# Kernel optimization log

Hardware: AMD Instinct MI355X
Metric: run time of the kernel (lower is better)

The kernel has to match this reference:

```python
import jax, jax.numpy as jnp
import numpy as np

D_MODEL = 1024
H = 16
DK = 64
DV = 64
EPS = 1e-5


def setup_inputs() -> dict:
    key = jax.random.key(0)
    ks = jax.random.split(key, 12)
    B, NQ, NK = 4, 2048, 2048
    std = 0.001  # init.normal_(weight, std=0.001), biases zero
    return {
        "queries": jax.random.normal(ks[0], (B, NQ, D_MODEL), jnp.float32),
        "keys": jax.random.normal(ks[1], (B, NK, D_MODEL), jnp.float32),
        "values": jax.random.normal(ks[2], (B, NK, D_MODEL), jnp.float32),
        "attention_mask": jnp.ones((B, NK), jnp.int32),  # 1 = keep
        "Wq": jax.random.normal(ks[3], (D_MODEL, H * DK), jnp.float32) * std,
        "bq": jnp.zeros((H * DK,), jnp.float32),
        "Wk": jax.random.normal(ks[4], (D_MODEL, H * DK), jnp.float32) * std,
        "bk": jnp.zeros((H * DK,), jnp.float32),
        "Wv": jax.random.normal(ks[5], (D_MODEL, H * DV), jnp.float32) * std,
        "bv": jnp.zeros((H * DV,), jnp.float32),
        "Wo": jax.random.normal(ks[6], (H * DV, D_MODEL), jnp.float32) * std,
        "bo": jnp.zeros((D_MODEL,), jnp.float32),
        "gamma": jnp.ones((D_MODEL,), jnp.float32),
        "beta": jnp.zeros((D_MODEL,), jnp.float32),
    }


def reference(queries, keys, values, attention_mask, Wq, bq, Wk, bk, Wv, bv, Wo, bo, gamma, beta):
    b, nq, _ = queries.shape
    nk = keys.shape[1]
    q = (queries @ Wq + bq).reshape(b, nq, H, DK)   # (b, nq, h, dk)
    k = (keys @ Wk + bk).reshape(b, nk, H, DK)      # (b, nk, h, dk)
    v = (values @ Wv + bv).reshape(b, nk, H, DV)    # (b, nk, h, dv)
    scale = 1.0 / np.sqrt(DK).astype(np.float32)
    att = jnp.einsum('bqhd,bkhd->bhqk', q, k) * scale  # (b, h, nq, nk)
    mask = attention_mask[:, None, None, :].astype(bool)
    att = jnp.where(mask, att, -jnp.inf)
    att = jax.nn.softmax(att, axis=-1)
    # dropout is identity at inference
    out = jnp.einsum('bhqk,bkhd->bqhd', att, v).reshape(b, nq, H * DV)
    out = out @ Wo + bo
    x = out + queries  # residual
    mean = jnp.mean(x, axis=-1, keepdims=True)
    var = jnp.mean(jnp.square(x - mean), axis=-1, keepdims=True)
    return gamma * (x - mean) * jax.lax.rsqrt(var + EPS) + beta
```

## Files before the change

### kernel.cpp

```cpp
#include <hip/hip_runtime.h>

typedef __bf16 bf16x8 __attribute__((ext_vector_type(8)));
typedef __bf16 bf16x4 __attribute__((ext_vector_type(4)));
typedef float f32x4 __attribute__((ext_vector_type(4)));
typedef unsigned short u16;

#if __has_builtin(__builtin_amdgcn_exp2f)
#define EXP2(x) __builtin_amdgcn_exp2f(x)
#else
#define EXP2(x) exp2f(x)
#endif

__device__ __forceinline__ float bf2f(u16 u){
    union { unsigned int i; float f; } x; x.i = ((unsigned int)u) << 16; return x.f;
}
__device__ __forceinline__ u16 f2bf(float f){
    union { float f; unsigned int i; } x; x.f = f;
    unsigned int r = x.i + 0x7fff + ((x.i >> 16) & 1);
    return (u16)(r >> 16);
}
__device__ __forceinline__ int4 cvt8(const float4 a, const float4 b){
    union { u16 h[8]; int4 v; } u;
    u.h[0] = f2bf(a.x); u.h[1] = f2bf(a.y); u.h[2] = f2bf(a.z); u.h[3] = f2bf(a.w);
    u.h[4] = f2bf(b.x); u.h[5] = f2bf(b.y); u.h[6] = f2bf(b.z); u.h[7] = f2bf(b.w);
    return u.v;
}

__global__ __launch_bounds__(256) void transpose4(
    const float* __restrict__ w0, const float* __restrict__ w1,
    const float* __restrict__ w2, const float* __restrict__ w3,
    u16* __restrict__ out)
{
    __shared__ float tile[32][33];
    int mat = blockIdx.z;
    const float* in = (mat == 0) ? w0 : (mat == 1) ? w1 : (mat == 2) ? w2 : w3;
    u16* o = out + (size_t)mat * 1048576;
    int bx = blockIdx.x * 32, by = blockIdx.y * 32;
    int tx = threadIdx.x & 31, ty = threadIdx.x >> 5;
    #pragma unroll
    for (int i = 0; i < 32; i += 8)
        tile[ty + i][tx] = in[(size_t)(by + ty + i) * 1024 + bx + tx];
    __syncthreads();
    #pragma unroll
    for (int i = 0; i < 32; i += 8)
        o[(size_t)(bx + ty + i) * 1024 + by + tx] = f2bf(tile[tx][ty + i]);
}

template<int MODE, bool AF32>
__global__ __launch_bounds__(256) void gemm_bt(
    const void* __restrict__ Av, const u16* __restrict__ Bt,
    const float* __restrict__ bias, const float* __restrict__ resid,
    void* __restrict__ Cv, float scale)
{
    constexpr int K = 1024;
    __shared__ alignas(16) u16 As[2][128][32];
    __shared__ alignas(16) u16 Bs[2][128][32];
    const int tid = threadIdx.x;
    const int lane = tid & 63, wid = tid >> 6;
    const int wm = wid >> 1, wn = wid & 1;
    const int m0 = blockIdx.x * 128, n0 = blockIdx.y * 128;
    const int r0 = tid >> 2;
    const int kc = (tid & 3) * 8;
    const int fr = lane & 15, fk = (lane >> 4) * 8;

    const float* Af0 = (const float*)Av + (size_t)(m0 + r0) * K + kc;
    const float* Af1 = Af0 + (size_t)64 * K;
    const u16*   Ah0 = (const u16*)Av + (size_t)(m0 + r0) * K + kc;
    const u16*   Ah1 = Ah0 + (size_t)64 * K;
    const u16* Brow0 = Bt + (size_t)(n0 + r0) * K + kc;
    const u16* Brow1 = Brow0 + (size_t)64 * K;

    int4 pa0, pa1, pb0, pb1;
    if constexpr (AF32) {
        pa0 = cvt8(((const float4*)Af0)[0], ((const float4*)Af0)[1]);
        pa1 = cvt8(((const float4*)Af1)[0], ((const float4*)Af1)[1]);
    } else {
        pa0 = *(const int4*)(Ah0);
        pa1 = *(const int4*)(Ah1);
    }
    pb0 = *(const int4*)(Brow0);
    pb1 = *(const int4*)(Brow1);
    *(int4*)&As[0][r0][kc]      = pa0;
    *(int4*)&As[0][r0 + 64][kc] = pa1;
    *(int4*)&Bs[0][r0][kc]      = pb0;
    *(int4*)&Bs[0][r0 + 64][kc] = pb1;
    __syncthreads();

    f32x4 acc[4][4] = {};
    constexpr int NT = K / 32;
    for (int t = 0; t < NT; ++t) {
        int cur = t & 1, nxt = cur ^ 1;
        if (t + 1 < NT) {
            if constexpr (AF32) {
                pa0 = cvt8(((const float4*)(Af0 + (t + 1) * 32))[0],
                           ((const float4*)(Af0 + (t + 1) * 32))[1]);
                pa1 = cvt8(((const float4*)(Af1 + (t + 1) * 32))[0],
                           ((const float4*)(Af1 + (t + 1) * 32))[1]);
            } else {
                pa0 = *(const int4*)(Ah0 + (t + 1) * 32);
                pa1 = *(const int4*)(Ah1 + (t + 1) * 32);
            }
            pb0 = *(const int4*)(Brow0 + (t + 1) * 32);
            pb1 = *(const int4*)(Brow1 + (t + 1) * 32);
        }
        bf16x8 af[4], bfr[4];
        #pragma unroll
        for (int i = 0; i < 4; i++) {
            af[i]  = *(const bf16x8*)&As[cur][wm * 64 + i * 16 + fr][fk];
            bfr[i] = *(const bf16x8*)&Bs[cur][wn * 64 + i * 16 + fr][fk];
        }
        #pragma unroll
        for (int mi = 0; mi < 4; mi++)
            #pragma unroll
            for (int ni = 0; ni < 4; ni++)
                acc[mi][ni] = __builtin_amdgcn_mfma_f32_16x16x32_bf16(
                    af[mi], bfr[ni], acc[mi][ni], 0, 0, 0);
        if (t + 1 < NT) {
            *(int4*)&As[nxt][r0][kc]      = pa0;
            *(int4*)&As[nxt][r0 + 64][kc] = pa1;
            *(int4*)&Bs[nxt][r0][kc]      = pb0;
            *(int4*)&Bs[nxt][r0 + 64][kc] = pb1;
        }
        __syncthreads();
    }

    #pragma unroll
    for (int ni = 0; ni < 4; ni++) {
        int col = n0 + wn * 64 + ni * 16 + fr;
        float bcol = bias[col];
        #pragma unroll
        for (int mi = 0; mi < 4; mi++) {
            #pragma unroll
            for (int r = 0; r < 4; r++) {
                int m = m0 + wm * 64 + mi * 16 + (lane >> 4) * 4 + r;
                float val = acc[mi][ni][r] + bcol;
                if (MODE == 2) {
                    val += resid[(size_t)m * 1024 + col];
                    ((float*)Cv)[(size_t)m * 1024 + col] = val;
                } else {
                    val *= scale;
                    int b = m >> 11, q = m & 2047;
                    int h = col >> 6, d = col & 63;
                    size_t base = (size_t)(b * 16 + h) * 131072;
                    if (MODE == 0) ((u16*)Cv)[base + (size_t)q * 64 + d] = f2bf(val);
                    else           ((u16*)Cv)[base + (size_t)d * 2048 + q] = f2bf(val);
                }
            }
        }
    }
}

__global__ __launch_bounds__(256) void attn_k(
    const u16* __restrict__ Qp, const u16* __restrict__ Kp,
    const u16* __restrict__ Vt, const int* __restrict__ mask,
    u16* __restrict__ O)
{
    __shared__ alignas(16) u16 Ks[2][64][64];
    __shared__ alignas(16) u16 Vs[2][64][64];
    __shared__ alignas(16) u16 Pl[4][16][64];

    const int wg = blockIdx.x;
    const int xc = wg & 7;
    const int rm = wg >> 3;
    const int qx = rm & 15;
    const int bh = (rm >> 4) * 8 + xc;
    const int b = bh >> 4, h = bh & 15;
    const int q0 = qx * 128;
    const int tid = threadIdx.x, wid = tid >> 6, lane = tid & 63;
    const int ql = lane & 15, g = lane >> 4;
    const int qw = q0 + wid * 32;

    const u16* Qbh = Qp + (size_t)bh * 131072;
    const u16* Kbh = Kp + (size_t)bh * 131072;
    const u16* Vbh = Vt + (size_t)bh * 131072;
    const int* mrow = mask + b * 2048;

    char* KsB0 = (char*)Ks;
    char* VsB0 = (char*)Vs;
    char* PlB = (char*)Pl + wid * 2048;

    bf16x8 qf[2][2];
    #pragma unroll
    for (int fi = 0; fi < 2; fi++)
        #pragma unroll
        for (int ks = 0; ks < 2; ks++)
            qf[fi][ks] = *(const bf16x8*)&Qbh[(size_t)(qw + fi * 16 + ql) * 64 + ks * 32 + g * 8];

    f32x4 oacc[2][4] = {};
    float lrow[2] = {0.f, 0.f};
    const f32x4 kZero = {0.f, 0.f, 0.f, 0.f};

    int pwoff[4], proff[2];
    #pragma unroll
    for (int kb = 0; kb < 4; kb++)
        pwoff[kb] = ql * 128 + ((kb * 32 + g * 8) ^ ((ql & 7) << 4));
    #pragma unroll
    for (int ks = 0; ks < 2; ks++)
        proff[ks] = ql * 128 + ((ks * 64 + g * 16) ^ ((ql & 7) << 4));

    const int sr  = tid >> 3;
    const int scb = (tid & 7) * 16;
    const int sw  = (sr & 7) << 4;

    int4 pk0, pk1, pv0, pv1;

    pk0 = *(const int4*)(Kbh + (size_t)sr * 64 + (tid & 7) * 8);
    pk1 = *(const int4*)(Kbh + (size_t)(sr + 32) * 64 + (tid & 7) * 8);
    pv0 = *(const int4*)(Vbh + (size_t)sr * 2048 + (tid & 7) * 8);
    pv1 = *(const int4*)(Vbh + (size_t)(sr + 32) * 2048 + (tid & 7) * 8);
    int mcur = mrow[lane];
    *(int4*)(KsB0 + sr * 128 + (scb ^ sw)) = pk0;
    *(int4*)(KsB0 + (sr + 32) * 128 + (scb ^ sw)) = pk1;
    *(int4*)(VsB0 + sr * 128 + (scb ^ sw)) = pv0;
    *(int4*)(VsB0 + (sr + 32) * 128 + (scb ^ sw)) = pv1;
    __syncthreads();

    for (int t = 0; t < 32; ++t) {
        const int cur = t & 1, nxt = cur ^ 1;
        char* KsB = KsB0 + cur * 8192;
        char* VsB = VsB0 + cur * 8192;
        int mnxt = 1;
        if (t < 31) {
            int kvn = (t + 1) * 64;
            pk0 = *(const int4*)(Kbh + (size_t)(kvn + sr) * 64 + (tid & 7) * 8);
            pk1 = *(const int4*)(Kbh + (size_t)(kvn + sr + 32) * 64 + (tid & 7) * 8);
            pv0 = *(const int4*)(Vbh + (size_t)sr * 2048 + kvn + (tid & 7) * 8);
            pv1 = *(const int4*)(Vbh + (size_t)(sr + 32) * 2048 + kvn + (tid & 7) * 8);
            mnxt = mrow[kvn + lane];
        }

        f32x4 s[2][4];
        __builtin_amdgcn_s_setprio(1);
        #pragma unroll
        for (int kb = 0; kb < 4; kb++) {
            int row = kb * 16 + ql;
            int swz = (row & 7) << 4;
            bf16x8 kf0 = *(const bf16x8*)(KsB + row * 128 + ((g * 16) ^ swz));
            bf16x8 kf1 = *(const bf16x8*)(KsB + row * 128 + ((64 + g * 16) ^ swz));
            #pragma unroll
            for (int fi = 0; fi < 2; fi++) {
                f32x4 a = __builtin_amdgcn_mfma_f32_16x16x32_bf16(kf0, qf[fi][0], kZero, 0, 0, 0);
                a = __builtin_amdgcn_mfma_f32_16x16x32_bf16(kf1, qf[fi][1], a, 0, 0, 0);
                s[fi][kb] = a;
            }
        }
        __builtin_amdgcn_s_setprio(0);

        if (__ballot(mcur == 0) != 0ull) {
            #pragma unroll
            for (int kb = 0; kb < 4; kb++) {
                int4 mi = *(const int4*)&mrow[t * 64 + kb * 16 + g * 4];
                f32x4 mv;
                mv[0] = mi.x ? 0.f : -1e30f;
                mv[1] = mi.y ? 0.f : -1e30f;
                mv[2] = mi.z ? 0.f : -1e30f;
                mv[3] = mi.w ? 0.f : -1e30f;
                #pragma unroll
                for (int fi = 0; fi < 2; fi++)
                    #pragma unroll
                    for (int r = 0; r < 4; r++) s[fi][kb][r] += mv[r];
            }
        }

        bf16x8 pf[2][2];
        #pragma unroll
        for (int fi = 0; fi < 2; fi++) {
            float ts[4];
            #pragma unroll
            for (int kb = 0; kb < 4; kb++) {
                float p0 = EXP2(s[fi][kb][0]);
                float p1 = EXP2(s[fi][kb][1]);
                float p2 = EXP2(s[fi][kb][2]);
                float p3 = EXP2(s[fi][kb][3]);
                ts[kb] = (p0 + p1) + (p2 + p3);
                bf16x4 pb;
                pb[0] = (__bf16)p0; pb[1] = (__bf16)p1;
                pb[2] = (__bf16)p2; pb[3] = (__bf16)p3;
                *(bf16x4*)(PlB + pwoff[kb]) = pb;
            }
            lrow[fi] += (ts[0] + ts[1]) + (ts[2] + ts[3]);
            #pragma unroll
            for (int ks = 0; ks < 2; ks++)
                pf[fi][ks] = *(const bf16x8*)(PlB + proff[ks]);
        }
        __builtin_amdgcn_s_setprio(1);
        #pragma unroll
        for (int dt = 0; dt < 4; dt++) {
            int row = dt * 16 + ql;
            int swz = (row & 7) << 4;
            bf16x8 vf0 = *(const bf16x8*)(VsB + row * 128 + ((g * 16) ^ swz));
            bf16x8 vf1 = *(const bf16x8*)(VsB + row * 128 + ((64 + g * 16) ^ swz));
            #pragma unroll
            for (int fi = 0; fi < 2; fi++) {
                oacc[fi][dt] = __builtin_amdgcn_mfma_f32_16x16x32_bf16(vf0, pf[fi][0], oacc[fi][dt], 0, 0, 0);
                oacc[fi][dt] = __builtin_amdgcn_mfma_f32_16x16x32_bf16(vf1, pf[fi][1], oacc[fi][dt], 0, 0, 0);
            }
        }
        __builtin_amdgcn_s_setprio(0);

        if (t < 31) {
            char* KsN = KsB0 + nxt * 8192;
            char* VsN = VsB0 + nxt * 8192;
            *(int4*)(KsN + sr * 128 + (scb ^ sw)) = pk0;
            *(int4*)(KsN + (sr + 32) * 128 + (scb ^ sw)) = pk1;
            *(int4*)(VsN + sr * 128 + (scb ^ sw)) = pv0;
            *(int4*)(VsN + (sr + 32) * 128 + (scb ^ sw)) = pv1;
        }
        mcur = mnxt;
        __syncthreads();
    }

    #pragma unroll
    for (int fi = 0; fi < 2; fi++) {
        lrow[fi] += __shfl_xor(lrow[fi], 16, 64);
        lrow[fi] += __shfl_xor(lrow[fi], 32, 64);
        float inv = 1.f / lrow[fi];
        #pragma unroll
        for (int dt = 0; dt < 4; dt++) {
            bf16x4 ob;
            ob[0] = (__bf16)(oacc[fi][dt][0] * inv);
            ob[1] = (__bf16)(oacc[fi][dt][1] * inv);
            ob[2] = (__bf16)(oacc[fi][dt][2] * inv);
            ob[3] = (__bf16)(oacc[fi][dt][3] * inv);
            *(bf16x4*)(PlB + ql * 128 + ((dt * 32 + g * 8) ^ ((ql & 7) << 4))) = ob;
        }
        int rr = lane >> 2;
        int q = qw + fi * 16 + rr;
        #pragma unroll
        for (int pass = 0; pass < 2; pass++) {
            int cc = (lane & 3) + pass * 4;
            int4 val = *(const int4*)(PlB + rr * 128 + ((cc * 16) ^ ((rr & 7) << 4)));
            *(int4*)&O[((size_t)(b * 2048 + q)) * 1024 + h * 64 + cc * 8] = val;
        }
    }
}

__global__ __launch_bounds__(256) void ln_k(
    const float* __restrict__ X, const float* __restrict__ gamma,
    const float* __restrict__ beta, float* __restrict__ out)
{
    const int row = blockIdx.x, tid = threadIdx.x;
    float4 v = ((const float4*)(X + (size_t)row * 1024))[tid];
    float s = v.x + v.y + v.z + v.w;
    float s2 = v.x * v.x + v.y * v.y + v.z * v.z + v.w * v.w;
    #pragma unroll
    for (int off = 1; off < 64; off <<= 1) {
        s  += __shfl_xor(s, off, 64);
        s2 += __shfl_xor(s2, off, 64);
    }
    __shared__ float ss[4], ss2[4];
    int wid = tid >> 6;
    if ((tid & 63) == 0) { ss[wid] = s; ss2[wid] = s2; }
    __syncthreads();
    s = ss[0] + ss[1] + ss[2] + ss[3];
    s2 = ss2[0] + ss2[1] + ss2[2] + ss2[3];
    float mean = s * (1.f / 1024.f);
    float var = s2 * (1.f / 1024.f) - mean * mean;
    float rstd = rsqrtf(var + 1e-5f);
    float4 g = ((const float4*)gamma)[tid];
    float4 be = ((const float4*)beta)[tid];
    float4 o;
    o.x = (v.x - mean) * rstd * g.x + be.x;
    o.y = (v.y - mean) * rstd * g.y + be.y;
    o.z = (v.z - mean) * rstd * g.z + be.z;
    o.w = (v.w - mean) * rstd * g.w + be.w;
    ((float4*)(out + (size_t)row * 1024))[tid] = o;
}

extern "C" void kernel_launch(void* const* d_in, const int* in_sizes, int n_in,
                              void* d_out, int out_size, void* d_ws, size_t ws_size,
                              hipStream_t stream)
{
    const float* queries = (const float*)d_in[0];
    const float* keys    = (const float*)d_in[1];
    const float* values  = (const float*)d_in[2];
    const int*   mask    = (const int*)d_in[3];
    const float* Wq = (const float*)d_in[4];
    const float* bq = (const float*)d_in[5];
    const float* Wk = (const float*)d_in[6];
    const float* bk = (const float*)d_in[7];
    const float* Wv = (const float*)d_in[8];
    const float* bv = (const float*)d_in[9];
    const float* Wo = (const float*)d_in[10];
    const float* bo = (const float*)d_in[11];
    const float* gamma = (const float*)d_in[12];
    const float* beta  = (const float*)d_in[13];

    u16* ws = (u16*)d_ws;
    u16* Wt = ws;
    u16* Qp = ws + 4 * 1048576;
    u16* Kp = Qp + 8388608;
    u16* Vt = Kp + 8388608;
    u16* O  = Vt + 8388608;
    float* X = (float*)Qp;

    const float qscale = 0.125f * 1.44269504088896f;

    transpose4<<<dim3(32, 32, 4), 256, 0, stream>>>(Wq, Wk, Wv, Wo, Wt);
    gemm_bt<0, true ><<<dim3(64, 8), 256, 0, stream>>>(queries, Wt,           bq, nullptr, Qp, qscale);
    gemm_bt<0, true ><<<dim3(64, 8), 256, 0, stream>>>(keys,    Wt + 1048576, bk, nullptr, Kp, 1.0f);
    gemm_bt<1, true ><<<dim3(64, 8), 256, 0, stream>>>(values,  Wt + 2097152, bv, nullptr, Vt, 1.0f);
    attn_k<<<dim3(1024), 256, 0, stream>>>(Qp, Kp, Vt, mask, O);
    gemm_bt<2, false><<<dim3(64, 8), 256, 0, stream>>>(O, Wt + 3145728, bo, queries, X, 1.0f);
    ln_k<<<8192, 256, 0, stream>>>(X, gamma, beta, (float*)d_out);
}
```

Baseline: 242.2 us.

## Stage K/V tiles with direct global-to-LDS loads and store pre-LN activations in bf16

The attention kernel now fills its double-buffered K/V shared-memory tiles with global_load_lds instructions that write straight into LDS. The swizzle is moved to the global source address, so the register round-trip and the separate LDS stores after the PV MFMAs are gone. Separately, the output projection writes the residual-added pre-LayerNorm tensor as bf16 instead of fp32, and the LayerNorm kernel reads bf16, roughly halving that intermediate traffic. This adds rounding error before normalization, and it relies on the async LDS writes being complete at the existing barrier without an explicit vmcnt wait.

```diff
diff --git a/kernel.cpp b/kernel.cpp
--- a/kernel.cpp
+++ b/kernel.cpp
@@ -24,6 +24,11 @@
     u.h[0] = f2bf(a.x); u.h[1] = f2bf(a.y); u.h[2] = f2bf(a.z); u.h[3] = f2bf(a.w);
     u.h[4] = f2bf(b.x); u.h[5] = f2bf(b.y); u.h[6] = f2bf(b.z); u.h[7] = f2bf(b.w);
     return u.v;
+}
+__device__ __forceinline__ void gload_lds16(const void* g, void* l){
+    __builtin_amdgcn_global_load_lds(
+        (const __attribute__((address_space(1))) unsigned int*)g,
+        (__attribute__((address_space(3))) unsigned int*)l, 16, 0, 0);
 }
 
 __global__ __launch_bounds__(256) void transpose4(
@@ -136,7 +141,7 @@
                 float val = acc[mi][ni][r] + bcol;
                 if (MODE == 2) {
                     val += resid[(size_t)m * 1024 + col];
-                    ((float*)Cv)[(size_t)m * 1024 + col] = val;
+                    ((u16*)Cv)[(size_t)m * 1024 + col] = f2bf(val);
                 } else {
                     val *= scale;
                     int b = m >> 11, q = m & 2047;
@@ -198,21 +203,24 @@
     for (int ks = 0; ks < 2; ks++)
         proff[ks] = ql * 128 + ((ks * 64 + g * 16) ^ ((ql & 7) << 4));
 
-    const int sr  = tid >> 3;
-    const int scb = (tid & 7) * 16;
-    const int sw  = (sr & 7) << 4;
-
-    int4 pk0, pk1, pv0, pv1;
-
-    pk0 = *(const int4*)(Kbh + (size_t)sr * 64 + (tid & 7) * 8);
-    pk1 = *(const int4*)(Kbh + (size_t)(sr + 32) * 64 + (tid & 7) * 8);
-    pv0 = *(const int4*)(Vbh + (size_t)sr * 2048 + (tid & 7) * 8);
-    pv1 = *(const int4*)(Vbh + (size_t)(sr + 32) * 2048 + (tid & 7) * 8);
+    const int lrow8 = lane >> 3;
+    const int coff  = ((lane & 7) ^ lrow8) << 4;
+    const int rb    = wid * 16;
+
+    auto stage = [&](int buf, int tt) {
+        const size_t kv0 = (size_t)tt * 64;
+        #pragma unroll
+        for (int i = 0; i < 2; i++) {
+            const int rt = rb + i * 8;
+            gload_lds16((const char*)Kbh + (kv0 + rt + lrow8) * 128 + coff,
+                        KsB0 + buf * 8192 + rt * 128);
+            gload_lds16((const char*)Vbh + (size_t)(rt + lrow8) * 4096 + kv0 * 2 + coff,
+                        VsB0 + buf * 8192 + rt * 128);
+        }
+    };
+
+    stage(0, 0);
     int mcur = mrow[lane];
-    *(int4*)(KsB0 + sr * 128 + (scb ^ sw)) = pk0;
-    *(int4*)(KsB0 + (sr + 32) * 128 + (scb ^ sw)) = pk1;
-    *(int4*)(VsB0 + sr * 128 + (scb ^ sw)) = pv0;
-    *(int4*)(VsB0 + (sr + 32) * 128 + (scb ^ sw)) = pv1;
     __syncthreads();
 
     for (int t = 0; t < 32; ++t) {
@@ -221,12 +229,8 @@
         char* VsB = VsB0 + cur * 8192;
         int mnxt = 1;
         if (t < 31) {
-            int kvn = (t + 1) * 64;
-            pk0 = *(const int4*)(Kbh + (size_t)(kvn + sr) * 64 + (tid & 7) * 8);
-            pk1 = *(const int4*)(Kbh + (size_t)(kvn + sr + 32) * 64 + (tid & 7) * 8);
-            pv0 = *(const int4*)(Vbh + (size_t)sr * 2048 + kvn + (tid & 7) * 8);
-            pv1 = *(const int4*)(Vbh + (size_t)(sr + 32) * 2048 + kvn + (tid & 7) * 8);
-            mnxt = mrow[kvn + lane];
+            stage(nxt, t + 1);
+            mnxt = mrow[(t + 1) * 64 + lane];
         }
 
         f32x4 s[2][4];
@@ -298,14 +302,6 @@
         }
         __builtin_amdgcn_s_setprio(0);
 
-        if (t < 31) {
-            char* KsN = KsB0 + nxt * 8192;
-            char* VsN = VsB0 + nxt * 8192;
-            *(int4*)(KsN + sr * 128 + (scb ^ sw)) = pk0;
-            *(int4*)(KsN + (sr + 32) * 128 + (scb ^ sw)) = pk1;
-            *(int4*)(VsN + sr * 128 + (scb ^ sw)) = pv0;
-            *(int4*)(VsN + (sr + 32) * 128 + (scb ^ sw)) = pv1;
-        }
         mcur = mnxt;
         __syncthreads();
     }
@@ -336,13 +332,14 @@
 }
 
 __global__ __launch_bounds__(256) void ln_k(
-    const float* __restrict__ X, const float* __restrict__ gamma,
+    const u16* __restrict__ X, const float* __restrict__ gamma,
     const float* __restrict__ beta, float* __restrict__ out)
 {
     const int row = blockIdx.x, tid = threadIdx.x;
-    float4 v = ((const float4*)(X + (size_t)row * 1024))[tid];
-    float s = v.x + v.y + v.z + v.w;
-    float s2 = v.x * v.x + v.y * v.y + v.z * v.z + v.w * v.w;
+    ushort4 u = ((const ushort4*)(X + (size_t)row * 1024))[tid];
+    float v0 = bf2f(u.x), v1 = bf2f(u.y), v2 = bf2f(u.z), v3 = bf2f(u.w);
+    float s = (v0 + v1) + (v2 + v3);
+    float s2 = (v0 * v0 + v1 * v1) + (v2 * v2 + v3 * v3);
     #pragma unroll
     for (int off = 1; off < 64; off <<= 1) {
         s  += __shfl_xor(s, off, 64);
@@ -357,13 +354,13 @@
     float mean = s * (1.f / 1024.f);
     float var = s2 * (1.f / 1024.f) - mean * mean;
     float rstd = rsqrtf(var + 1e-5f);
-    float4 g = ((const float4*)gamma)[tid];
+    float4 gm = ((const float4*)gamma)[tid];
     float4 be = ((const float4*)beta)[tid];
     float4 o;
-    o.x = (v.x - mean) * rstd * g.x + be.x;
-    o.y = (v.y - mean) * rstd * g.y + be.y;
-    o.z = (v.z - mean) * rstd * g.z + be.z;
-    o.w = (v.w - mean) * rstd * g.w + be.w;
+    o.x = (v0 - mean) * rstd * gm.x + be.x;
+    o.y = (v1 - mean) * rstd * gm.y + be.y;
+    o.z = (v2 - mean) * rstd * gm.z + be.z;
+    o.w = (v3 - mean) * rstd * gm.w + be.w;
     ((float4*)(out + (size_t)row * 1024))[tid] = o;
 }
 
@@ -392,7 +389,7 @@
     u16* Kp = Qp + 8388608;
     u16* Vt = Kp + 8388608;
     u16* O  = Vt + 8388608;
-    float* X = (float*)Qp;
+    u16* X  = Qp;
 
     const float qscale = 0.125f * 1.44269504088896f;
 
```

Result: no change. 240.0 us (-0.9%).
